# Kernel optimization log

Hardware: AMD Instinct MI355X
Metric: run time of the kernel (lower is better)

The kernel has to match this reference:

```python
import jax, jax.numpy as jnp
import numpy as np

BN_EPS = 1e-5
K = 16


def pairwise_sqdist(a, b):
    # a: (B,N,C), b: (B,M,C) -> (B,N,M)
    aa = jnp.sum(a * a, axis=-1)[:, :, None]
    bb = jnp.sum(b * b, axis=-1)[:, None, :]
    return aa + bb - 2.0 * jnp.einsum('bnc,bmc->bnm', a, b)


def knn_idx(pts, k):
    # pts: (B,N,C) -> (B,N,k) indices of k nearest points (incl. self)
    d = pairwise_sqdist(pts, pts)
    _, idx = jax.lax.top_k(-d, k)
    return idx


def gather_points(pts, idx):
    # pts: (B,N,C), idx: (B,N,k) -> (B,N,k,C)
    return jax.vmap(lambda p, i: p[i])(pts, idx)


def conv_bn(x, W, b, gm, bt, relu=True):
    # 1x1 Conv1d + BatchNorm1d (training-mode batch stats) [+ ReLU]
    # x: (B,Cin,N), W: (Cout,Cin)
    y = jnp.einsum('oc,bcn->bon', W, x) + b[None, :, None]
    mu = jnp.mean(y, axis=(0, 2), keepdims=True)
    var = jnp.var(y, axis=(0, 2), keepdims=True)
    y = (y - mu) / jnp.sqrt(var + BN_EPS) * gm[None, :, None] + bt[None, :, None]
    return jax.nn.relu(y) if relu else y


def graph_layer(x, W, b, gm, bt):
    # x: (B,C,N)
    ft = jnp.swapaxes(x, 1, 2)                # (B,N,C)
    idx = knn_idx(ft, K)                      # (B,N,k)
    knn_x = gather_points(ft, idx)            # (B,N,k,C)
    m = jnp.max(knn_x, axis=2)                # (B,N,C)
    return conv_bn(jnp.swapaxes(m, 1, 2), W, b, gm, bt, relu=True)


def setup_inputs() -> dict:
    key = jax.random.key(0)
    ks = jax.random.split(key, 8)
    B, N = 8, 2048
    d = {'x': jax.random.normal(ks[0], (B, N, 3), dtype=jnp.float32)}

    def conv_params(k, cout, cin):
        W = jax.random.normal(k, (cout, cin), dtype=jnp.float32) * 0.02
        return W, jnp.zeros((cout,), jnp.float32), jnp.ones((cout,), jnp.float32), jnp.zeros((cout,), jnp.float32)

    for name, k, co, ci in [('1', ks[1], 64, 12), ('2', ks[2], 64, 64), ('3', ks[3], 64, 64),
                            ('g1', ks[4], 128, 64), ('g2', ks[5], 1024, 128), ('4', ks[6], 512, 1024)]:
        W, b, gm, bt = conv_params(k, co, ci)
        d['W' + name] = W; d['b' + name] = b; d['gm' + name] = gm; d['bt' + name] = bt
    return d


def reference(x, W1, b1, gm1, bt1, W2, b2, gm2, bt2, W3, b3, gm3, bt3,
              Wg1, bg1, gmg1, btg1, Wg2, bg2, gmg2, btg2, W4, b4, gm4, bt4):
    # x: (B,N,3)
    idx = knn_idx(x, K)                       # (B,N,k)
    knn_x = gather_points(x, idx)             # (B,N,k,3)
    knn_x = knn_x - jnp.mean(knn_x, axis=2, keepdims=True)
    cov = jnp.einsum('bnkc,bnkd->bncd', knn_x, knn_x)      # (B,N,3,3)
    B, N = x.shape[0], x.shape[1]
    cov = cov.reshape(B, N, 9).transpose(0, 2, 1)          # (B,9,N)
    h = jnp.concatenate([jnp.swapaxes(x, 1, 2), cov], axis=1)  # (B,12,N)
    h = conv_bn(h, W1, b1, gm1, bt1)
    h = conv_bn(h, W2, b2, gm2, bt2)
    h = conv_bn(h, W3, b3, gm3, bt3)
    h = graph_layer(h, Wg1, bg1, gmg1, btg1)               # (B,128,N)
    h = graph_layer(h, Wg2, bg2, gmg2, btg2)               # (B,1024,N)
    h = conv_bn(h, W4, b4, gm4, bt4, relu=False)           # (B,512,N)
    return jnp.max(h, axis=-1)                             # (B,512)
```

## Files before the change

kernel.cpp:

```cpp
#include <hip/hip_runtime.h>
#include <math.h>

#define B_ 8
#define N_ 2048
#define KNN 16

typedef __attribute__((ext_vector_type(4))) float f32x4;
typedef __attribute__((ext_vector_type(8))) short bf16x8;
typedef __attribute__((ext_vector_type(8))) _Float16 f16x8;
typedef __attribute__((address_space(3))) unsigned int lds_u32_t;
typedef __attribute__((address_space(1))) const unsigned int glb_u32_t;

__device__ inline unsigned short f2bf(float f) {
    unsigned int x = __float_as_uint(f);
    unsigned int r = (x + 0x7fffu + ((x >> 16) & 1u)) >> 16;
    return (unsigned short)r;
}

__device__ inline unsigned int fflip(float f) {
    unsigned int u = __float_as_uint(f);
    return u ^ (0x80000000u | (unsigned int)((int)u >> 31));
}

__device__ inline unsigned long long shflx64(unsigned long long v, int m) {
    int lo = __shfl_xor((int)(unsigned int)(v & 0xffffffffull), m, 64);
    int hi = __shfl_xor((int)(unsigned int)(v >> 32), m, 64);
    return ((unsigned long long)(unsigned int)hi << 32) | (unsigned int)lo;
}

__device__ inline void ce(unsigned long long& a, unsigned long long& b) {
    bool c = a < b;
    unsigned long long lo = c ? a : b;
    unsigned long long hi = c ? b : a;
    a = lo;
    b = hi;
}

#define SORT16(q)                                                         \
    _Pragma("unroll") for (int kk_ = 2; kk_ <= 16; kk_ <<= 1)             \
    _Pragma("unroll") for (int jj_ = kk_ >> 1; jj_ > 0; jj_ >>= 1)        \
    _Pragma("unroll") for (int ii_ = 0; ii_ < 16; ii_++) {                \
        int ll_ = ii_ ^ jj_;                                              \
        if (ll_ > ii_) {                                                  \
            if ((ii_ & kk_) == 0) ce(q[ii_], q[ll_]);                     \
            else ce(q[ll_], q[ii_]);                                      \
        }                                                                 \
    }

#define MERGE16(q)                                                        \
    _Pragma("unroll") for (int jj_ = 8; jj_ > 0; jj_ >>= 1)               \
    _Pragma("unroll") for (int ii_ = 0; ii_ < 16; ii_++) {                \
        int ll_ = ii_ ^ jj_;                                              \
        if (ll_ > ii_) ce(q[ii_], q[ll_]);                                \
    }

#define TOP16OF32(kA, kB, q)                                              \
    SORT16(kA);                                                           \
    SORT16(kB);                                                           \
    _Pragma("unroll") for (int ii_ = 0; ii_ < 16; ii_++) {                \
        unsigned long long b_ = kB[15 - ii_];                             \
        q[ii_] = kA[ii_] < b_ ? kA[ii_] : b_;                             \
    }                                                                     \
    MERGE16(q);

#define EXTRACT16(q, op)                                                  \
    for (int r_ = 0; r_ < KNN; r_++) {                                    \
        unsigned long long mk_ = q[0];                                    \
        _Pragma("unroll") for (int s_ = 32; s_ > 0; s_ >>= 1) {           \
            unsigned long long ok_ = shflx64(mk_, s_);                    \
            if (ok_ < mk_) mk_ = ok_;                                     \
        }                                                                 \
        if (lane == 0) (op)[r_] = (int)(mk_ & 2047u);                     \
        bool pop_ = (q[0] == mk_);                                        \
        _Pragma("unroll") for (int t_ = 0; t_ < 15; t_++)                 \
            q[t_] = pop_ ? q[t_ + 1] : q[t_];                             \
        q[15] = pop_ ? ~0ull : q[15];                                     \
    }

__global__ __launch_bounds__(256, 4) void knn3_kernel(const float* __restrict__ x,
                                                      int* __restrict__ idx,
                                                      float* __restrict__ h0) {
    __shared__ float px[N_], py[N_], pz[N_];
    int b = blockIdx.y;
    const float* xb = x + (size_t)b * N_ * 3;
    for (int e = threadIdx.x; e < N_; e += 256) {
        px[e] = xb[e * 3 + 0];
        py[e] = xb[e * 3 + 1];
        pz[e] = xb[e * 3 + 2];
    }
    __syncthreads();

    int wave = threadIdx.x >> 6, lane = threadIdx.x & 63;
    int i = blockIdx.x * 4 + wave;
    float qx = px[i], qy = py[i], qz = pz[i];

    unsigned long long kA[16], kB[16];
#pragma unroll
    for (int t = 0; t < 16; t++) {
        int j = lane + t * 64;
        float dx = px[j] - qx, dy = py[j] - qy, dz = pz[j] - qz;
        float d = dx * dx + dy * dy + dz * dz;
        kA[t] = ((unsigned long long)fflip(d) << 11) | (unsigned int)j;
    }
#pragma unroll
    for (int t = 0; t < 16; t++) {
        int j = lane + (t + 16) * 64;
        float dx = px[j] - qx, dy = py[j] - qy, dz = pz[j] - qz;
        float d = dx * dx + dy * dy + dz * dz;
        kB[t] = ((unsigned long long)fflip(d) << 11) | (unsigned int)j;
    }

    unsigned long long q[16];
    TOP16OF32(kA, kB, q);

    int* op = idx + ((size_t)b * N_ + i) * KNN;
    unsigned int jr[16];
#pragma unroll
    for (int r_ = 0; r_ < KNN; r_++) {
        unsigned long long mk_ = q[0];
#pragma unroll
        for (int s_ = 32; s_ > 0; s_ >>= 1) {
            unsigned long long ok_ = shflx64(mk_, s_);
            if (ok_ < mk_) mk_ = ok_;
        }
        jr[r_] = (unsigned int)(mk_ & 2047u);
        if (lane == 0) op[r_] = (int)jr[r_];
        bool pop_ = (q[0] == mk_);
#pragma unroll
        for (int t_ = 0; t_ < 15; t_++) q[t_] = pop_ ? q[t_ + 1] : q[t_];
        q[15] = pop_ ? ~0ull : q[15];
    }

    float nx[16], ny[16], nz[16];
    float mx = 0.f, my = 0.f, mz = 0.f;
#pragma unroll
    for (int r_ = 0; r_ < 16; r_++) {
        int j = (int)jr[r_];
        nx[r_] = px[j]; ny[r_] = py[j]; nz[r_] = pz[j];
        mx += nx[r_]; my += ny[r_]; mz += nz[r_];
    }
    mx *= (1.f / KNN); my *= (1.f / KNN); mz *= (1.f / KNN);
    float c00 = 0, c01 = 0, c02 = 0, c11 = 0, c12 = 0, c22 = 0;
#pragma unroll
    for (int r_ = 0; r_ < 16; r_++) {
        float dx = nx[r_] - mx, dy = ny[r_] - my, dz = nz[r_] - mz;
        c00 += dx * dx; c01 += dx * dy; c02 += dx * dz;
        c11 += dy * dy; c12 += dy * dz; c22 += dz * dz;
    }
    if (lane == 0) {
        float* hb = h0 + (size_t)b * 12 * N_;
        hb[0 * N_ + i] = qx;
        hb[1 * N_ + i] = qy;
        hb[2 * N_ + i] = qz;
        hb[3 * N_ + i] = c00; hb[4 * N_ + i] = c01; hb[5 * N_ + i] = c02;
        hb[6 * N_ + i] = c01; hb[7 * N_ + i] = c11; hb[8 * N_ + i] = c12;
        hb[9 * N_ + i] = c02; hb[10 * N_ + i] = c12; hb[11 * N_ + i] = c22;
    }
}

__global__ __launch_bounds__(256) void gemm_kernel(const float* __restrict__ A,
                                                   const float* __restrict__ X,
                                                   const float* __restrict__ bias,
                                                   float* __restrict__ Y,
                                                   int O, int C) {
    __shared__ float Wt[16][132];
    __shared__ float Xt[16][132];
    const int N = N_;
    int b = blockIdx.z;
    int oB = blockIdx.y * 128, nB = blockIdx.x * 128;
    const float* Xb = X + (size_t)b * C * N;
    int tid = threadIdx.x;
    int tn = tid & 15, to = tid >> 4;

    float acc[8][8];
#pragma unroll
    for (int i = 0; i < 8; i++)
#pragma unroll
        for (int j = 0; j < 8; j++) acc[i][j] = 0.f;

    for (int c0 = 0; c0 < C; c0 += 16) {
#pragma unroll
        for (int r = 0; r < 8; r++) {
            int e = tid + r * 256;
            int k = e & 15, o = e >> 4;
            float v = 0.f;
            if (c0 + k < C && oB + o < O) v = A[(size_t)(oB + o) * C + c0 + k];
            Wt[k][o] = v;
        }
#pragma unroll
        for (int r = 0; r < 8; r++) {
            int e = tid + r * 256;
            int n = e & 127, k = e >> 7;
            float v = 0.f;
            if (c0 + k < C) v = Xb[(size_t)(c0 + k) * N + nB + n];
            Xt[k][n] = v;
        }
        __syncthreads();
#pragma unroll
        for (int k = 0; k < 16; k++) {
            float a[8], xv[8];
#pragma unroll
            for (int i = 0; i < 8; i++) a[i] = Wt[k][to * 8 + i];
#pragma unroll
            for (int m = 0; m < 4; m++) {
                xv[2 * m] = Xt[k][tn * 2 + 32 * m];
                xv[2 * m + 1] = Xt[k][tn * 2 + 32 * m + 1];
            }
#pragma unroll
            for (int i = 0; i < 8; i++)
#pragma unroll
                for (int j = 0; j < 8; j++) acc[i][j] = fmaf(a[i], xv[j], acc[i][j]);
        }
        __syncthreads();
    }

#pragma unroll
    for (int i = 0; i < 8; i++) {
        int o = oB + to * 8 + i;
        if (o >= O) continue;
        float bv = bias[o];
#pragma unroll
        for (int m = 0; m < 4; m++) {
            int n0 = nB + tn * 2 + 32 * m;
            float2 st = make_float2(acc[i][2 * m] + bv, acc[i][2 * m + 1] + bv);
            *reinterpret_cast<float2*>(&Y[((size_t)b * O + o) * N + n0]) = st;
        }
    }
}

__global__ __launch_bounds__(256) void splitbn_kernel(const float* __restrict__ y,
                                                      const float* __restrict__ scale,
                                                      const float* __restrict__ shift,
                                                      _Float16* __restrict__ fh,
                                                      _Float16* __restrict__ fl, int O) {
    __shared__ float tile[64][65];
    int b = blockIdx.z;
    int n0 = blockIdx.x * 64, o0 = blockIdx.y * 64;
    int t = threadIdx.x;
#pragma unroll
    for (int rr = 0; rr < 16; rr++) {
        int ol = rr * 4 + (t >> 6), nl = t & 63;
        float v = y[((size_t)b * O + o0 + ol) * N_ + n0 + nl];
        v = fmaf(v, scale[o0 + ol], shift[o0 + ol]);
        tile[ol][nl] = fmaxf(v, 0.f);
    }
    __syncthreads();
#pragma unroll
    for (int rr = 0; rr < 2; rr++) {
        int e = t + rr * 256;
        int n = e >> 3, og = (e & 7) * 8;
        f16x8 hv, lv;
#pragma unroll
        for (int j = 0; j < 8; j++) {
            float v = tile[og + j][n];
            _Float16 h = (_Float16)v;
            hv[j] = h;
            lv[j] = (_Float16)(v - (float)h);
        }
        size_t off = ((size_t)b * N_ + n0 + n) * O + o0 + og;
        *reinterpret_cast<uint4*>(&fh[off]) = *reinterpret_cast<uint4*>(&hv);
        *reinterpret_cast<uint4*>(&fl[off]) = *reinterpret_cast<uint4*>(&lv);
    }
}

__global__ __launch_bounds__(256) void normsh_kernel(const _Float16* __restrict__ fh,
                                                     const _Float16* __restrict__ fl,
                                                     float* __restrict__ nrm, int C) {
    int b = blockIdx.y;
    int i = blockIdx.x * 256 + threadIdx.x;
    const _Float16* ph = fh + ((size_t)(b << 11) + i) * C;
    const _Float16* pl = fl + ((size_t)(b << 11) + i) * C;
    float s = 0.f;
    for (int c = 0; c < C; c += 8) {
        f16x8 h = *reinterpret_cast<const f16x8*>(&ph[c]);
        f16x8 l = *reinterpret_cast<const f16x8*>(&pl[c]);
#pragma unroll
        for (int q = 0; q < 8; q++) {
            float v = (float)h[q] + (float)l[q];
            s = fmaf(v, v, s);
        }
    }
    nrm[(b << 11) + i] = s;
}

__global__ __launch_bounds__(256) void dmfma_kernel(const _Float16* __restrict__ Fh,
                                                    const _Float16* __restrict__ Fl,
                                                    const float* __restrict__ nrm,
                                                    float* __restrict__ D, int C) {
    __shared__ __align__(16) char smem[65536];
    _Float16* Ah = (_Float16*)(smem);
    _Float16* Al = (_Float16*)(smem + 16384);
    _Float16* Bh = (_Float16*)(smem + 32768);
    _Float16* Bl = (_Float16*)(smem + 49152);
    float(*Tt)[132] = (float(*)[132])smem;

    int bz = blockIdx.z;
    int t = blockIdx.x;
    int bx = (int)((sqrtf(8.f * (float)t + 1.f) - 1.f) * 0.5f);
    while ((bx + 1) * (bx + 2) / 2 <= t) bx++;
    while (bx * (bx + 1) / 2 > t) bx--;
    int by = t - bx * (bx + 1) / 2;
    int oB = by * 128, nB = bx * 128;
    const _Float16* Fhb = Fh + (size_t)bz * N_ * C;
    const _Float16* Flb = Fl + (size_t)bz * N_ * C;
    const float* nb = nrm + (size_t)bz * N_;
    float* Db = D + (size_t)bz * N_ * N_;

    int tid = threadIdx.x;
    int lane = tid & 63, w = tid >> 6;
    int wm = w & 1, wn = w >> 1;
    int lr = lane & 15, lg = lane >> 4;
    int lrow = lane >> 3;
    int lcol = ((lane & 7) ^ lrow) * 8;

    f32x4 acc[4][4];
#pragma unroll
    for (int m = 0; m < 4; m++)
#pragma unroll
        for (int n = 0; n < 4; n++) acc[m][n] = (f32x4){0.f, 0.f, 0.f, 0.f};

    for (int c0 = 0; c0 < C; c0 += 64) {
#pragma unroll
        for (int r = 0; r < 4; r++) {
            int seg = r * 4 + w;
            int row = seg * 8 + lrow;
            const _Float16* gah = &Fhb[(size_t)(oB + row) * C + c0 + lcol];
            const _Float16* gal = &Flb[(size_t)(oB + row) * C + c0 + lcol];
            const _Float16* gbh = &Fhb[(size_t)(nB + row) * C + c0 + lcol];
            const _Float16* gbl = &Flb[(size_t)(nB + row) * C + c0 + lcol];
            __builtin_amdgcn_global_load_lds((glb_u32_t*)gah, (lds_u32_t*)&Ah[seg * 512], 16, 0, 0);
            __builtin_amdgcn_global_load_lds((glb_u32_t*)gal, (lds_u32_t*)&Al[seg * 512], 16, 0, 0);
            __builtin_amdgcn_global_load_lds((glb_u32_t*)gbh, (lds_u32_t*)&Bh[seg * 512], 16, 0, 0);
            __builtin_amdgcn_global_load_lds((glb_u32_t*)gbl, (lds_u32_t*)&Bl[seg * 512], 16, 0, 0);
        }
        __syncthreads();
#pragma unroll
        for (int kk = 0; kk < 2; kk++) {
            f16x8 ah[4], al[4], bh[4], bl[4];
#pragma unroll
            for (int m = 0; m < 4; m++) {
                int row = wm * 64 + m * 16 + lr;
                int slot = (kk * 4 + lg) ^ (lr & 7);
                ah[m] = *reinterpret_cast<const f16x8*>(&Ah[row * 64 + slot * 8]);
                al[m] = *reinterpret_cast<const f16x8*>(&Al[row * 64 + slot * 8]);
            }
#pragma unroll
            for (int n = 0; n < 4; n++) {
                int row = wn * 64 + n * 16 + lr;
                int slot = (kk * 4 + lg) ^ (lr & 7);
                bh[n] = *reinterpret_cast<const f16x8*>(&Bh[row * 64 + slot * 8]);
                bl[n] = *reinterpret_cast<const f16x8*>(&Bl[row * 64 + slot * 8]);
            }
#pragma unroll
            for (int m = 0; m < 4; m++)
#pragma unroll
                for (int n = 0; n < 4; n++) {
                    acc[m][n] = __builtin_amdgcn_mfma_f32_16x16x32_f16(al[m], bh[n], acc[m][n], 0, 0, 0);
                    acc[m][n] = __builtin_amdgcn_mfma_f32_16x16x32_f16(ah[m], bl[n], acc[m][n], 0, 0, 0);
                    acc[m][n] = __builtin_amdgcn_mfma_f32_16x16x32_f16(ah[m], bh[n], acc[m][n], 0, 0, 0);
                }
        }
        __syncthreads();
    }

#pragma unroll
    for (int m = 0; m < 4; m++) {
#pragma unroll
        for (int r = 0; r < 4; r++) {
            int o = oB + wm * 64 + m * 16 + lg * 4 + r;
            float nr_ = nb[o];
#pragma unroll
            for (int n = 0; n < 4; n++) {
                int nv = nB + wn * 64 + n * 16 + lr;
                float val = nr_ + nb[nv] - 2.f * acc[m][n][r];
                unsigned int fk = fflip(val);
                Db[(size_t)o * N_ + nv] = __uint_as_float(fk);
                acc[m][n][r] = __uint_as_float(fk);
            }
        }
    }

    if (bx != by) {
        for (int p = 0; p < 4; p++) {
            __syncthreads();
            if (wm == (p >> 1)) {
#pragma unroll
                for (int mh = 0; mh < 2; mh++) {
                    int m = (p & 1) * 2 + mh;
                    int ib = m * 16 + lg * 4 - (p & 1) * 32;
#pragma unroll
                    for (int n = 0; n < 4; n++) {
                        int j = wn * 64 + n * 16 + lr;
#pragma unroll
                        for (int r = 0; r < 4; r++) Tt[ib + r][j] = acc[m][n][r];
                    }
                }
            }
            __syncthreads();
#pragma unroll
            for (int r = 0; r < 4; r++) {
                int e = tid + r * 256;
                int j = e >> 3, i4 = e & 7;
                float4 v;
                v.x = Tt[i4 * 4 + 0][j];
                v.y = Tt[i4 * 4 + 1][j];
                v.z = Tt[i4 * 4 + 2][j];
                v.w = Tt[i4 * 4 + 3][j];
                *reinterpret_cast<float4*>(&Db[(size_t)(nB + j) * N_ + oB + p * 32 + i4 * 4]) = v;
            }
        }
    }
}

template <int XLAYOUT, int FUSE, int DUALT>
__global__ __launch_bounds__(256, 4) void cgemm_kernel(const float* __restrict__ A,
                                                       const float* __restrict__ X,
                                                       const float* __restrict__ bias,
                                                       float* __restrict__ Y,
                                                       int O, int C,
                                                       const float* __restrict__ xs,
                                                       const float* __restrict__ xh,
                                                       float* __restrict__ Yt) {
    __shared__ float Wt[32][68];
    __shared__ float Xt[32][68];
    int b = blockIdx.z;
    int oB = blockIdx.y * 64, nB = blockIdx.x * 64;
    const float* Xb = X + (XLAYOUT == 0 ? (size_t)b * C * N_ : (size_t)b * N_ * C);
    int tid = threadIdx.x;
    int tn = tid & 15, to = tid >> 4;

    float acc[4][4];
#pragma unroll
    for (int i = 0; i < 4; i++)
#pragma unroll
        for (int j = 0; j < 4; j++) acc[i][j] = 0.f;

    for (int c0 = 0; c0 < C; c0 += 32) {
#pragma unroll
        for (int r = 0; r < 2; r++) {
            int e = tid + r * 256;
            int row = e >> 3, c4 = e & 7;
            float4 v = *reinterpret_cast<const float4*>(&A[(size_t)(oB + row) * C + c0 + c4 * 4]);
            Wt[c4 * 4 + 0][row] = v.x;
            Wt[c4 * 4 + 1][row] = v.y;
            Wt[c4 * 4 + 2][row] = v.z;
            Wt[c4 * 4 + 3][row] = v.w;
        }
        if (XLAYOUT == 0) {
#pragma unroll
            for (int r = 0; r < 2; r++) {
                int e = tid + r * 256;
                int k = e >> 4, n4 = e & 15;
                float4 v = *reinterpret_cast<const float4*>(&Xb[(size_t)(c0 + k) * N_ + nB + n4 * 4]);
                if (FUSE) {
                    float sc = xs[c0 + k], sh = xh[c0 + k];
                    v.x = fmaxf(fmaf(v.x, sc, sh), 0.f);
                    v.y = fmaxf(fmaf(v.y, sc, sh), 0.f);
                    v.z = fmaxf(fmaf(v.z, sc, sh), 0.f);
                    v.w = fmaxf(fmaf(v.w, sc, sh), 0.f);
                }
                *reinterpret_cast<float4*>(&Xt[k][n4 * 4]) = v;
            }
        } else {
#pragma unroll
            for (int r = 0; r < 2; r++) {
                int e = tid + r * 256;
                int n = e >> 3, c4 = e & 7;
                float4 v = *reinterpret_cast<const float4*>(&Xb[(size_t)(nB + n) * C + c0 + c4 * 4]);
                Xt[c4 * 4 + 0][n] = v.x;
                Xt[c4 * 4 + 1][n] = v.y;
                Xt[c4 * 4 + 2][n] = v.z;
                Xt[c4 * 4 + 3][n] = v.w;
            }
        }
        __syncthreads();
#pragma unroll
        for (int k = 0; k < 32; k++) {
            float a[4], xv[4];
            *reinterpret_cast<float4*>(&a[0]) = *reinterpret_cast<const float4*>(&Wt[k][to * 4]);
            *reinterpret_cast<float4*>(&xv[0]) = *reinterpret_cast<const float4*>(&Xt[k][tn * 4]);
#pragma unroll
            for (int i = 0; i < 4; i++)
#pragma unroll
                for (int j = 0; j < 4; j++) acc[i][j] = fmaf(a[i], xv[j], acc[i][j]);
        }
        __syncthreads();
    }

    float fin[4][4];
#pragma unroll
    for (int i = 0; i < 4; i++) {
        float bv = bias[oB + to * 4 + i];
#pragma unroll
        for (int j = 0; j < 4; j++) fin[i][j] = acc[i][j] + bv;
    }
#pragma unroll
    for (int i = 0; i < 4; i++) {
        int o = oB + to * 4 + i;
        int n0 = nB + tn * 4;
        float4 st;
        st.x = fin[i][0]; st.y = fin[i][1]; st.z = fin[i][2]; st.w = fin[i][3];
        *reinterpret_cast<float4*>(&Y[((size_t)b * O + o) * N_ + n0]) = st;
    }
    if (DUALT) {
#pragma unroll
        for (int j = 0; j < 4; j++) {
            int n = nB + tn * 4 + j;
            float4 st;
            st.x = fin[0][j]; st.y = fin[1][j]; st.z = fin[2][j]; st.w = fin[3][j];
            *reinterpret_cast<float4*>(&Yt[((size_t)b * N_ + n) * (size_t)O + oB + to * 4]) = st;
        }
    }
}

template <int EPI>
__global__ __launch_bounds__(256) void mgemm_kernel(const unsigned short* __restrict__ A,
                                                    const unsigned short* __restrict__ X,
                                                    const float* __restrict__ bias,
                                                    float* __restrict__ Y,
                                                    int O, int C,
                                                    float* __restrict__ part) {
    __shared__ unsigned short At[128 * 64];
    __shared__ unsigned short Bt[128 * 64];
    __shared__ float sred[2][2][64][4];
    int b = blockIdx.z;
    int oB = blockIdx.y * 128, nB = blockIdx.x * 128;
    const unsigned short* Xb = X + (size_t)b * N_ * C;
    int tid = threadIdx.x;
    int lane = tid & 63, w = tid >> 6;
    int wm = w & 1, wn = w >> 1;
    int lr = lane & 15, lg = lane >> 4;
    int lrow = lane >> 3;
    int lcol = ((lane & 7) ^ lrow) * 8;

    f32x4 acc[4][4];
#pragma unroll
    for (int m = 0; m < 4; m++)
#pragma unroll
        for (int n = 0; n < 4; n++) acc[m][n] = (f32x4){0.f, 0.f, 0.f, 0.f};

    for (int c0 = 0; c0 < C; c0 += 64) {
#pragma unroll
        for (int r = 0; r < 4; r++) {
            int seg = r * 4 + w;
            int row = seg * 8 + lrow;
            const unsigned short* ga = &A[(size_t)(oB + row) * C + c0 + lcol];
            const unsigned short* gb = &Xb[(size_t)(nB + row) * C + c0 + lcol];
            __builtin_amdgcn_global_load_lds((glb_u32_t*)ga, (lds_u32_t*)&At[seg * 512], 16, 0, 0);
            __builtin_amdgcn_global_load_lds((glb_u32_t*)gb, (lds_u32_t*)&Bt[seg * 512], 16, 0, 0);
        }
        __syncthreads();
#pragma unroll
        for (int kk = 0; kk < 2; kk++) {
            bf16x8 af[4], bfv[4];
#pragma unroll
            for (int m = 0; m < 4; m++) {
                int row = wm * 64 + m * 16 + lr;
                int slot = (kk * 4 + lg) ^ (lr & 7);
                af[m] = *reinterpret_cast<const bf16x8*>(&At[row * 64 + slot * 8]);
            }
#pragma unroll
            for (int n = 0; n < 4; n++) {
                int row = wn * 64 + n * 16 + lr;
                int slot = (kk * 4 + lg) ^ (lr & 7);
                bfv[n] = *reinterpret_cast<const bf16x8*>(&Bt[row * 64 + slot * 8]);
            }
#pragma unroll
            for (int m = 0; m < 4; m++)
#pragma unroll
                for (int n = 0; n < 4; n++)
                    acc[m][n] = __builtin_amdgcn_mfma_f32_16x16x32_bf16(af[m], bfv[n], acc[m][n], 0, 0, 0);
        }
        __syncthreads();
    }

    if (EPI == 1) {
#pragma unroll
        for (int m = 0; m < 4; m++) {
#pragma unroll
            for (int r = 0; r < 4; r++) {
                float v0 = acc[m][0][r], v1 = acc[m][1][r];
                float v2 = acc[m][2][r], v3 = acc[m][3][r];
                float mx = fmaxf(fmaxf(v0, v1), fmaxf(v2, v3));
                float mn = fminf(fminf(v0, v1), fminf(v2, v3));
                float s = (v0 + v1) + (v2 + v3);
                float s2 = fmaf(v0, v0, fmaf(v1, v1, fmaf(v2, v2, v3 * v3)));
#pragma unroll
                for (int msk = 1; msk <= 8; msk <<= 1) {
                    mx = fmaxf(mx, __shfl_xor(mx, msk, 64));
                    mn = fminf(mn, __shfl_xor(mn, msk, 64));
                    s += __shfl_xor(s, msk, 64);
                    s2 += __shfl_xor(s2, msk, 64);
                }
                if (lr == 0) {
                    int ol = m * 16 + lg * 4 + r;
                    sred[wm][wn][ol][0] = mx;
                    sred[wm][wn][ol][1] = mn;
                    sred[wm][wn][ol][2] = s;
                    sred[wm][wn][ol][3] = s2;
                }
            }
        }
        __syncthreads();
        if (tid < 128) {
            int wmv = tid >> 6, ol = tid & 63;
            float mx = fmaxf(sred[wmv][0][ol][0], sred[wmv][1][ol][0]);
            float mn = fminf(sred[wmv][0][ol][1], sred[wmv][1][ol][1]);
            float s = sred[wmv][0][ol][2] + sred[wmv][1][ol][2];
            float s2 = sred[wmv][0][ol][3] + sred[wmv][1][ol][3];
            int o = oB + wmv * 64 + ol;
            float* pp = &part[((size_t)(o * 8 + b) * 16 + blockIdx.x) * 4];
            pp[0] = mx; pp[1] = mn; pp[2] = s; pp[3] = s2;
        }
    } else {
#pragma unroll
        for (int m = 0; m < 4; m++) {
            int o0 = oB + wm * 64 + m * 16 + lg * 4;
            float4 bv = *reinterpret_cast<const float4*>(&bias[o0]);
            float s[4] = {0.f, 0.f, 0.f, 0.f};
            float s2[4] = {0.f, 0.f, 0.f, 0.f};
#pragma unroll
            for (int n = 0; n < 4; n++) {
                int nv = nB + wn * 64 + n * 16 + lr;
                float4 st;
                st.x = acc[m][n][0] + bv.x;
                st.y = acc[m][n][1] + bv.y;
                st.z = acc[m][n][2] + bv.z;
                st.w = acc[m][n][3] + bv.w;
                *reinterpret_cast<float4*>(&Y[((size_t)b * N_ + nv) * (size_t)O + o0]) = st;
                s[0] += st.x; s2[0] = fmaf(st.x, st.x, s2[0]);
                s[1] += st.y; s2[1] = fmaf(st.y, st.y, s2[1]);
                s[2] += st.z; s2[2] = fmaf(st.z, st.z, s2[2]);
                s[3] += st.w; s2[3] = fmaf(st.w, st.w, s2[3]);
            }
#pragma unroll
            for (int r = 0; r < 4; r++) {
#pragma unroll
                for (int msk = 1; msk <= 8; msk <<= 1) {
                    s[r] += __shfl_xor(s[r], msk, 64);
                    s2[r] += __shfl_xor(s2[r], msk, 64);
                }
                if (lr == 0) {
                    int ol = m * 16 + lg * 4 + r;
                    sred[wm][wn][ol][0] = s[r];
                    sred[wm][wn][ol][1] = s2[r];
                }
            }
        }
        __syncthreads();
        if (tid < 128) {
            int wmv = tid >> 6, ol = tid & 63;
            float s = sred[wmv][0][ol][0] + sred[wmv][1][ol][0];
            float s2 = sred[wmv][0][ol][1] + sred[wmv][1][ol][1];
            int o = oB + wmv * 64 + ol;
            float* pp = &part[((size_t)(o * 8 + b) * 16 + blockIdx.x) * 2];
            pp[0] = s; pp[1] = s2;
        }
    }
}

__global__ __launch_bounds__(128) void bnfin_kernel(const float* __restrict__ part,
                                                    const float* __restrict__ gm,
                                                    const float* __restrict__ bt,
                                                    float* __restrict__ scale,
                                                    float* __restrict__ shift) {
    int o = blockIdx.x;
    int t = threadIdx.x;
    const float* p = &part[((size_t)(o * 8 + (t >> 4)) * 16 + (t & 15)) * 2];
    float s = p[0], s2 = p[1];
#pragma unroll
    for (int msk = 1; msk <= 32; msk <<= 1) {
        s += __shfl_xor(s, msk, 64);
        s2 += __shfl_xor(s2, msk, 64);
    }
    __shared__ float red[4];
    int wv = t >> 6, lane = t & 63;
    if (lane == 0) { red[wv] = s; red[2 + wv] = s2; }
    __syncthreads();
    if (t == 0) {
        float S = red[0] + red[1], S2 = red[2] + red[3];
        float mu = S * (1.f / (B_ * N_));
        float var = S2 * (1.f / (B_ * N_)) - mu * mu;
        float inv = 1.f / sqrtf(var + 1e-5f);
        float sc = gm[o] * inv;
        scale[o] = sc;
        shift[o] = fmaf(-mu, sc, bt[o]);
    }
}

__global__ __launch_bounds__(256) void applycvt_kernel(const float* __restrict__ yt,
                                                       const float* __restrict__ scale,
                                                       const float* __restrict__ shift,
                                                       unsigned short* __restrict__ outh) {
    size_t i = ((size_t)blockIdx.x * 256 + threadIdx.x) * 8;
    int o = (int)(i & 1023u);
    float4 a = *reinterpret_cast<const float4*>(&yt[i]);
    float4 c = *reinterpret_cast<const float4*>(&yt[i + 4]);
    float4 s0 = *reinterpret_cast<const float4*>(&scale[o]);
    float4 s1 = *reinterpret_cast<const float4*>(&scale[o + 4]);
    float4 h0 = *reinterpret_cast<const float4*>(&shift[o]);
    float4 h1 = *reinterpret_cast<const float4*>(&shift[o + 4]);
    unsigned short u[8];
    u[0] = f2bf(fmaxf(fmaf(a.x, s0.x, h0.x), 0.f));
    u[1] = f2bf(fmaxf(fmaf(a.y, s0.y, h0.y), 0.f));
    u[2] = f2bf(fmaxf(fmaf(a.z, s0.z, h0.z), 0.f));
    u[3] = f2bf(fmaxf(fmaf(a.w, s0.w, h0.w), 0.f));
    u[4] = f2bf(fmaxf(fmaf(c.x, s1.x, h1.x), 0.f));
    u[5] = f2bf(fmaxf(fmaf(c.y, s1.y, h1.y), 0.f));
    u[6] = f2bf(fmaxf(fmaf(c.z, s1.z, h1.z), 0.f));
    u[7] = f2bf(fmaxf(fmaf(c.w, s1.w, h1.w), 0.f));
    uint4 pk;
    pk.x = (unsigned)u[0] | ((unsigned)u[1] << 16);
    pk.y = (unsigned)u[2] | ((unsigned)u[3] << 16);
    pk.z = (unsigned)u[4] | ((unsigned)u[5] << 16);
    pk.w = (unsigned)u[6] | ((unsigned)u[7] << 16);
    *reinterpret_cast<uint4*>(&outh[i]) = pk;
}

__global__ __launch_bounds__(128) void bnmax_kernel(const float* __restrict__ part,
                                                    const float* __restrict__ gm,
                                                    const float* __restrict__ bt,
                                                    float* __restrict__ out) {
    int o = blockIdx.x;
    int t = threadIdx.x;
    int b = t >> 4, nb = t & 15;
    const float* p = &part[((size_t)(o * 8 + b) * 16 + nb) * 4];
    float mx = p[0], mn = p[1], s = p[2], s2 = p[3];

    float ss = s, ss2 = s2;
#pragma unroll
    for (int msk = 1; msk <= 32; msk <<= 1) {
        ss += __shfl_xor(ss, msk, 64);
        ss2 += __shfl_xor(ss2, msk, 64);
    }
    __shared__ float red[4];
    int wv = t >> 6, lane = t & 63;
    if (lane == 0) { red[wv] = ss; red[2 + wv] = ss2; }
    __syncthreads();
    float S = red[0] + red[1], S2 = red[2] + red[3];
    float mu = S * (1.f / (B_ * N_));
    float var = S2 * (1.f / (B_ * N_)) - mu * mu;
    float inv = 1.f / sqrtf(var + 1e-5f);
    float sc = gm[o] * inv;
    float sh = fmaf(-mu, sc, bt[o]);

#pragma unroll
    for (int msk = 1; msk <= 8; msk <<= 1) {
        mx = fmaxf(mx, __shfl_xor(mx, msk, 64));
        mn = fminf(mn, __shfl_xor(mn, msk, 64));
    }
    if (nb == 0) out[b * 512 + o] = fmaf(sc, sc >= 0.f ? mx : mn, sh);
}

__global__ __launch_bounds__(256) void bnstats_kernel(const float* __restrict__ y,
                                                      const float* __restrict__ gm,
                                                      const float* __restrict__ bt,
                                                      float* __restrict__ scale,
                                                      float* __restrict__ shift, int O) {
    int o = blockIdx.x;
    float s = 0.f, s2 = 0.f;
    for (int e = threadIdx.x; e < B_ * N_; e += 256) {
        int b = e >> 11, n = e & (N_ - 1);
        float v = y[((size_t)b * O + o) * N_ + n];
        s += v;
        s2 = fmaf(v, v, s2);
    }
#pragma unroll
    for (int off = 32; off; off >>= 1) {
        s += __shfl_down(s, off, 64);
        s2 += __shfl_down(s2, off, 64);
    }
    __shared__ float red[8];
    int lane = threadIdx.x & 63, w = threadIdx.x >> 6;
    if (lane == 0) { red[w] = s; red[4 + w] = s2; }
    __syncthreads();
    if (threadIdx.x == 0) {
        s = red[0] + red[1] + red[2] + red[3];
        s2 = red[4] + red[5] + red[6] + red[7];
        float mu = s * (1.f / (B_ * N_));
        float var = s2 * (1.f / (B_ * N_)) - mu * mu;
        float inv = 1.f / sqrtf(var + 1e-5f);
        float sc = gm[o] * inv;
        scale[o] = sc;
        shift[o] = fmaf(-mu, sc, bt[o]);
    }
}

__global__ __launch_bounds__(256, 4) void topk_kernel(const float* __restrict__ D,
                                                      int* __restrict__ idx) {
    int wave = threadIdx.x >> 6, lane = threadIdx.x & 63;
    int i = blockIdx.x * 4 + wave;
    const unsigned int* dp = (const unsigned int*)(D + (size_t)i * N_);

    unsigned long long kA[16], kB[16];
#pragma unroll
    for (int t = 0; t < 4; t++) {
        uint4 v = *reinterpret_cast<const uint4*>(&dp[t * 256 + lane * 4]);
        int j0 = t * 256 + lane * 4;
        kA[t * 4 + 0] = ((unsigned long long)v.x << 11) | (unsigned int)(j0 + 0);
        kA[t * 4 + 1] = ((unsigned long long)v.y << 11) | (unsigned int)(j0 + 1);
        kA[t * 4 + 2] = ((unsigned long long)v.z << 11) | (unsigned int)(j0 + 2);
        kA[t * 4 + 3] = ((unsigned long long)v.w << 11) | (unsigned int)(j0 + 3);
    }
#pragma unroll
    for (int t = 4; t < 8; t++) {
        uint4 v = *reinterpret_cast<const uint4*>(&dp[t * 256 + lane * 4]);
        int j0 = t * 256 + lane * 4;
        kB[(t - 4) * 4 + 0] = ((unsigned long long)v.x << 11) | (unsigned int)(j0 + 0);
        kB[(t - 4) * 4 + 1] = ((unsigned long long)v.y << 11) | (unsigned int)(j0 + 1);
        kB[(t - 4) * 4 + 2] = ((unsigned long long)v.z << 11) | (unsigned int)(j0 + 2);
        kB[(t - 4) * 4 + 3] = ((unsigned long long)v.w << 11) | (unsigned int)(j0 + 3);
    }

    unsigned long long q[16];
    TOP16OF32(kA, kB, q);

    int* op = idx + (size_t)i * KNN;
    EXTRACT16(q, op);
}

__global__ __launch_bounds__(256) void gathermax_kernel(const float* __restrict__ ftraw,
                                                        const int* __restrict__ idx,
                                                        const float* __restrict__ scale,
                                                        const float* __restrict__ shift,
                                                        float* __restrict__ out, int cLog) {
    int C = 1 << cLog;
    int b = blockIdx.y;
    int nb = (blockIdx.x << (8 - cLog)) + (threadIdx.x >> cLog);
    int c = threadIdx.x & (C - 1);
    float sc = scale[c], sh = shift[c];
    const int* ip = idx + (((size_t)b << 11) + nb) * KNN;
    float m = -3.4e38f;
#pragma unroll
    for (int k = 0; k < KNN; k++) {
        int j = ip[k];
        float v = ftraw[(((size_t)b << 11) + j) * C + c];
        m = fmaxf(m, fmaxf(fmaf(v, sc, sh), 0.f));
    }
    out[(((size_t)b << 11) + nb) * C + c] = m;
}

__global__ __launch_bounds__(256) void gmaxh2_kernel(const float* __restrict__ ftraw,
                                                     const int* __restrict__ idx,
                                                     const float* __restrict__ scale,
                                                     const float* __restrict__ shift,
                                                     unsigned short* __restrict__ out) {
    const int C = 128;
    int b = blockIdx.y;
    int nb = blockIdx.x * 16 + (threadIdx.x >> 4);
    int cc = (threadIdx.x & 15) * 8;
    float4 s0 = *reinterpret_cast<const float4*>(&scale[cc]);
    float4 s1 = *reinterpret_cast<const float4*>(&scale[cc + 4]);
    float4 h0 = *reinterpret_cast<const float4*>(&shift[cc]);
    float4 h1 = *reinterpret_cast<const float4*>(&shift[cc + 4]);
    const int* ip = idx + (((size_t)b << 11) + nb) * KNN;
    float m[8];
#pragma unroll
    for (int q = 0; q < 8; q++) m[q] = -3.4e38f;
#pragma unroll
    for (int k = 0; k < KNN; k++) {
        int j = ip[k];
        const float* p = &ftraw[(((size_t)b << 11) + j) * C + cc];
        float4 a = *reinterpret_cast<const float4*>(p);
        float4 c2 = *reinterpret_cast<const float4*>(p + 4);
        m[0] = fmaxf(m[0], fmaxf(fmaf(a.x, s0.x, h0.x), 0.f));
        m[1] = fmaxf(m[1], fmaxf(fmaf(a.y, s0.y, h0.y), 0.f));
        m[2] = fmaxf(m[2], fmaxf(fmaf(a.z, s0.z, h0.z), 0.f));
        m[3] = fmaxf(m[3], fmaxf(fmaf(a.w, s0.w, h0.w), 0.f));
        m[4] = fmaxf(m[4], fmaxf(fmaf(c2.x, s1.x, h1.x), 0.f));
        m[5] = fmaxf(m[5], fmaxf(fmaf(c2.y, s1.y, h1.y), 0.f));
        m[6] = fmaxf(m[6], fmaxf(fmaf(c2.z, s1.z, h1.z), 0.f));
        m[7] = fmaxf(m[7], fmaxf(fmaf(c2.w, s1.w, h1.w), 0.f));
    }
    unsigned short u[8];
#pragma unroll
    for (int q = 0; q < 8; q++) u[q] = f2bf(m[q]);
    uint4 pk;
    pk.x = (unsigned)u[0] | ((unsigned)u[1] << 16);
    pk.y = (unsigned)u[2] | ((unsigned)u[3] << 16);
    pk.z = (unsigned)u[4] | ((unsigned)u[5] << 16);
    pk.w = (unsigned)u[6] | ((unsigned)u[7] << 16);
    *reinterpret_cast<uint4*>(&out[(((size_t)b << 11) + nb) * C + cc]) = pk;
}

__global__ __launch_bounds__(256) void wcvt2_kernel(const float* __restrict__ w1,
                                                    unsigned short* __restrict__ o1, int c1,
                                                    const float* __restrict__ w2,
                                                    unsigned short* __restrict__ o2, int c2) {
    int i = blockIdx.x * 256 + threadIdx.x;
    if (i < c1) o1[i] = f2bf(w1[i]);
    else if (i < c1 + c2) o2[i - c1] = f2bf(w2[i - c1]);
}

extern "C" void kernel_launch(void* const* d_in, const int* in_sizes, int n_in,
                              void* d_out, int out_size, void* d_ws, size_t ws_size,
                              hipStream_t stream) {
    const float* x = (const float*)d_in[0];
    const float* W1 = (const float*)d_in[1];
    const float* b1 = (const float*)d_in[2];
    const float* gm1 = (const float*)d_in[3];
    const float* bt1 = (const float*)d_in[4];
    const float* W2 = (const float*)d_in[5];
    const float* b2 = (const float*)d_in[6];
    const float* gm2 = (const float*)d_in[7];
    const float* bt2 = (const float*)d_in[8];
    const float* W3 = (const float*)d_in[9];
    const float* b3 = (const float*)d_in[10];
    const float* gm3 = (const float*)d_in[11];
    const float* bt3 = (const float*)d_in[12];
    const float* Wg1 = (const float*)d_in[13];
    const float* bg1 = (const float*)d_in[14];
    const float* gmg1 = (const float*)d_in[15];
    const float* btg1 = (const float*)d_in[16];
    const float* Wg2 = (const float*)d_in[17];
    const float* bg2 = (const float*)d_in[18];
    const float* gmg2 = (const float*)d_in[19];
    const float* btg2 = (const float*)d_in[20];
    const float* W4 = (const float*)d_in[21];
    const float* b4 = (const float*)d_in[22];
    const float* gm4 = (const float*)d_in[23];
    const float* bt4 = (const float*)d_in[24];
    float* out = (float*)d_out;
    (void)b4;

    if (ws_size < 154214400ull) return;
    char* base = (char*)d_ws;
    float* scale = (float*)(base + 0);
    float* shift = (float*)(base + 4096);
    float* nrm = (float*)(base + 8192);
    int* idx = (int*)(base + 73728);
    unsigned short* Wg2h = (unsigned short*)(base + 1122304);
    unsigned short* W4h = (unsigned short*)(base + 1384448);
    _Float16* Fh1 = (_Float16*)(base + 2433024);
    _Float16* Fl1 = (_Float16*)(base + 4530176);
    _Float16* Fh2 = (_Float16*)(base + 6627328);
    _Float16* Fl2 = (_Float16*)(base + 10821632);
    float* bufD4 = (float*)(base + 19210240);
    float* bufLt = (float*)(base + 19210240);
    unsigned short* bufLh = (unsigned short*)(base + 86319104);
    char* E = base + 119873536;
    float* h0 = (float*)(E + 0);
    float* bufA = (float*)(E + 786432);
    float* bufB = (float*)(E + 4980736);
    float* bufC = (float*)(E + 9175040);
    float* bufM1 = (float*)(E + 13369344);
    float* bufM2 = (float*)(E + 21757952);
    unsigned short* bufM3h = (unsigned short*)(E + 30146560);
    float* part = (float*)(E + 0);

    wcvt2_kernel<<<2560, 256, 0, stream>>>(Wg2, Wg2h, 1024 * 128, W4, W4h, 512 * 1024);

    knn3_kernel<<<dim3(512, 8), 256, 0, stream>>>(x, idx, h0);

    gemm_kernel<<<dim3(16, 1, 8), 256, 0, stream>>>(W1, h0, b1, bufA, 64, 12);
    bnstats_kernel<<<64, 256, 0, stream>>>(bufA, gm1, bt1, scale, shift, 64);

    cgemm_kernel<0, 1, 0><<<dim3(32, 1, 8), 256, 0, stream>>>(W2, bufA, b2, bufB, 64, 64, scale, shift, nullptr);
    bnstats_kernel<<<64, 256, 0, stream>>>(bufB, gm2, bt2, scale, shift, 64);

    cgemm_kernel<0, 1, 1><<<dim3(32, 1, 8), 256, 0, stream>>>(W3, bufB, b3, bufA, 64, 64, scale, shift, bufC);
    bnstats_kernel<<<64, 256, 0, stream>>>(bufA, gm3, bt3, scale, shift, 64);

    splitbn_kernel<<<dim3(32, 1, 8), 256, 0, stream>>>(bufA, scale, shift, Fh1, Fl1, 64);
    normsh_kernel<<<dim3(8, 8), 256, 0, stream>>>(Fh1, Fl1, nrm, 64);
    for (int c = 0; c < 2; c++) {
        dmfma_kernel<<<dim3(136, 1, 4), 256, 0, stream>>>(
            Fh1 + (size_t)c * 4 * N_ * 64, Fl1 + (size_t)c * 4 * N_ * 64,
            nrm + (size_t)c * 4 * N_, bufD4, 64);
        topk_kernel<<<2048, 256, 0, stream>>>(bufD4, idx + (size_t)c * 4 * N_ * KNN);
    }
    gathermax_kernel<<<dim3(512, 8), 256, 0, stream>>>(bufC, idx, scale, shift, bufB, 6);

    cgemm_kernel<1, 0, 1><<<dim3(32, 2, 8), 256, 0, stream>>>(Wg1, bufB, bg1, bufM1, 128, 64, nullptr, nullptr, bufM2);
    bnstats_kernel<<<128, 256, 0, stream>>>(bufM1, gmg1, btg1, scale, shift, 128);

    splitbn_kernel<<<dim3(32, 2, 8), 256, 0, stream>>>(bufM1, scale, shift, Fh2, Fl2, 128);
    normsh_kernel<<<dim3(8, 8), 256, 0, stream>>>(Fh2, Fl2, nrm, 128);
    for (int c = 0; c < 2; c++) {
        dmfma_kernel<<<dim3(136, 1, 4), 256, 0, stream>>>(
            Fh2 + (size_t)c * 4 * N_ * 128, Fl2 + (size_t)c * 4 * N_ * 128,
            nrm + (size_t)c * 4 * N_, bufD4, 128);
        topk_kernel<<<2048, 256, 0, stream>>>(bufD4, idx + (size_t)c * 4 * N_ * KNN);
    }
    gmaxh2_kernel<<<dim3(128, 8), 256, 0, stream>>>(bufM2, idx, scale, shift, bufM3h);

    mgemm_kernel<2><<<dim3(16, 8, 8), 256, 0, stream>>>(Wg2h, bufM3h, bg2, bufLt, 1024, 128, part);
    bnfin_kernel<<<1024, 128, 0, stream>>>(part, gmg2, btg2, scale, shift);
    applycvt_kernel<<<8192, 256, 0, stream>>>(bufLt, scale, shift, bufLh);

    mgemm_kernel<1><<<dim3(16, 4, 8), 256, 0, stream>>>(W4h, bufLh, nullptr, nullptr, 512, 1024, part);
    bnmax_kernel<<<512, 128, 0, stream>>>(part, gm4, bt4, out);
}
```

Baseline: 515.6 us.

## Fuse BN partial statistics into GEMM epilogues and batch first kNN distance pass

The GEMM and cgemm epilogues now emit per-block partial sums and sums of squares, and small finalize kernels (bnfin, new bnfin32) replace the bnstats kernels that reread the whole output. The first graph layer's distance GEMM and top-k now run once over all 8 batches instead of in two halves of 4, using a larger D buffer, and bufC moves to a new workspace region to make room. This removes full-tensor rereads for batch-norm statistics and two kernel launches, at the cost of more workspace and extra shuffles in the epilogues.

```diff
diff --git a/kernel.cpp b/kernel.cpp
--- a/kernel.cpp
+++ b/kernel.cpp
@@ -162,7 +162,8 @@
                                                    const float* __restrict__ X,
                                                    const float* __restrict__ bias,
                                                    float* __restrict__ Y,
-                                                   int O, int C) {
+                                                   int O, int C,
+                                                   float* __restrict__ part) {
     __shared__ float Wt[16][132];
     __shared__ float Xt[16][132];
     const int N = N_;
@@ -219,11 +220,23 @@
         int o = oB + to * 8 + i;
         if (o >= O) continue;
         float bv = bias[o];
+        float s = 0.f, s2 = 0.f;
 #pragma unroll
         for (int m = 0; m < 4; m++) {
             int n0 = nB + tn * 2 + 32 * m;
-            float2 st = make_float2(acc[i][2 * m] + bv, acc[i][2 * m + 1] + bv);
-            *reinterpret_cast<float2*>(&Y[((size_t)b * O + o) * N + n0]) = st;
+            float v0 = acc[i][2 * m] + bv, v1 = acc[i][2 * m + 1] + bv;
+            *reinterpret_cast<float2*>(&Y[((size_t)b * O + o) * N + n0]) = make_float2(v0, v1);
+            s += v0 + v1;
+            s2 = fmaf(v0, v0, fmaf(v1, v1, s2));
+        }
+#pragma unroll
+        for (int msk = 1; msk <= 8; msk <<= 1) {
+            s += __shfl_xor(s, msk, 64);
+            s2 += __shfl_xor(s2, msk, 64);
+        }
+        if (tn == 0) {
+            float* pp = &part[((size_t)(o * 8 + b) * 16 + blockIdx.x) * 2];
+            pp[0] = s; pp[1] = s2;
         }
     }
 }
@@ -420,7 +433,8 @@
                                                        int O, int C,
                                                        const float* __restrict__ xs,
                                                        const float* __restrict__ xh,
-                                                       float* __restrict__ Yt) {
+                                                       float* __restrict__ Yt,
+                                                       float* __restrict__ part) {
     __shared__ float Wt[32][68];
     __shared__ float Xt[32][68];
     int b = blockIdx.z;
@@ -509,6 +523,22 @@
             float4 st;
             st.x = fin[0][j]; st.y = fin[1][j]; st.z = fin[2][j]; st.w = fin[3][j];
             *reinterpret_cast<float4*>(&Yt[((size_t)b * N_ + n) * (size_t)O + oB + to * 4]) = st;
+        }
+    }
+#pragma unroll
+    for (int i = 0; i < 4; i++) {
+        float s = (fin[i][0] + fin[i][1]) + (fin[i][2] + fin[i][3]);
+        float s2 = fmaf(fin[i][0], fin[i][0], fmaf(fin[i][1], fin[i][1],
+                   fmaf(fin[i][2], fin[i][2], fin[i][3] * fin[i][3])));
+#pragma unroll
+        for (int msk = 1; msk <= 8; msk <<= 1) {
+            s += __shfl_xor(s, msk, 64);
+            s2 += __shfl_xor(s2, msk, 64);
+        }
+        if (tn == 0) {
+            int o = oB + to * 4 + i;
+            float* pp = &part[((size_t)(o * 8 + b) * 32 + blockIdx.x) * 2];
+            pp[0] = s; pp[1] = s2;
         }
     }
 }
@@ -679,6 +709,36 @@
     __syncthreads();
     if (t == 0) {
         float S = red[0] + red[1], S2 = red[2] + red[3];
+        float mu = S * (1.f / (B_ * N_));
+        float var = S2 * (1.f / (B_ * N_)) - mu * mu;
+        float inv = 1.f / sqrtf(var + 1e-5f);
+        float sc = gm[o] * inv;
+        scale[o] = sc;
+        shift[o] = fmaf(-mu, sc, bt[o]);
+    }
+}
+
+__global__ __launch_bounds__(256) void bnfin32_kernel(const float* __restrict__ part,
+                                                      const float* __restrict__ gm,
+                                                      const float* __restrict__ bt,
+                                                      float* __restrict__ scale,
+                                                      float* __restrict__ shift) {
+    int o = blockIdx.x;
+    int t = threadIdx.x;
+    const float* p = &part[((size_t)(o * 8 + (t >> 5)) * 32 + (t & 31)) * 2];
+    float s = p[0], s2 = p[1];
+#pragma unroll
+    for (int msk = 1; msk <= 32; msk <<= 1) {
+        s += __shfl_xor(s, msk, 64);
+        s2 += __shfl_xor(s2, msk, 64);
+    }
+    __shared__ float red[8];
+    int wv = t >> 6, lane = t & 63;
+    if (lane == 0) { red[wv] = s; red[4 + wv] = s2; }
+    __syncthreads();
+    if (t == 0) {
+        float S = (red[0] + red[1]) + (red[2] + red[3]);
+        float S2 = (red[4] + red[5]) + (red[6] + red[7]);
         float mu = S * (1.f / (B_ * N_));
         float var = S2 * (1.f / (B_ * N_)) - mu * mu;
         float inv = 1.f / sqrtf(var + 1e-5f);
@@ -750,40 +810,6 @@
         mn = fminf(mn, __shfl_xor(mn, msk, 64));
     }
     if (nb == 0) out[b * 512 + o] = fmaf(sc, sc >= 0.f ? mx : mn, sh);
-}
-
-__global__ __launch_bounds__(256) void bnstats_kernel(const float* __restrict__ y,
-                                                      const float* __restrict__ gm,
-                                                      const float* __restrict__ bt,
-                                                      float* __restrict__ scale,
-                                                      float* __restrict__ shift, int O) {
-    int o = blockIdx.x;
-    float s = 0.f, s2 = 0.f;
-    for (int e = threadIdx.x; e < B_ * N_; e += 256) {
-        int b = e >> 11, n = e & (N_ - 1);
-        float v = y[((size_t)b * O + o) * N_ + n];
-        s += v;
-        s2 = fmaf(v, v, s2);
-    }
-#pragma unroll
-    for (int off = 32; off; off >>= 1) {
-        s += __shfl_down(s, off, 64);
-        s2 += __shfl_down(s2, off, 64);
-    }
-    __shared__ float red[8];
-    int lane = threadIdx.x & 63, w = threadIdx.x >> 6;
-    if (lane == 0) { red[w] = s; red[4 + w] = s2; }
-    __syncthreads();
-    if (threadIdx.x == 0) {
-        s = red[0] + red[1] + red[2] + red[3];
-        s2 = red[4] + red[5] + red[6] + red[7];
-        float mu = s * (1.f / (B_ * N_));
-        float var = s2 * (1.f / (B_ * N_)) - mu * mu;
-        float inv = 1.f / sqrtf(var + 1e-5f);
-        float sc = gm[o] * inv;
-        scale[o] = sc;
-        shift[o] = fmaf(-mu, sc, bt[o]);
-    }
 }
 
 __global__ __launch_bounds__(256, 4) void topk_kernel(const float* __restrict__ D,
@@ -928,6 +954,7 @@
     float* scale = (float*)(base + 0);
     float* shift = (float*)(base + 4096);
     float* nrm = (float*)(base + 8192);
+    float* partC1 = (float*)(base + 8192);
     int* idx = (int*)(base + 73728);
     unsigned short* Wg2h = (unsigned short*)(base + 1122304);
     unsigned short* W4h = (unsigned short*)(base + 1384448);
@@ -935,14 +962,16 @@
     _Float16* Fl1 = (_Float16*)(base + 4530176);
     _Float16* Fh2 = (_Float16*)(base + 6627328);
     _Float16* Fl2 = (_Float16*)(base + 10821632);
+    float* bufC = (float*)(base + 15015936);
+    float* bufD8 = (float*)(base + 19210240);
     float* bufD4 = (float*)(base + 19210240);
     float* bufLt = (float*)(base + 19210240);
     unsigned short* bufLh = (unsigned short*)(base + 86319104);
     char* E = base + 119873536;
+    float* partC = (float*)(E + 0);
     float* h0 = (float*)(E + 0);
     float* bufA = (float*)(E + 786432);
     float* bufB = (float*)(E + 4980736);
-    float* bufC = (float*)(E + 9175040);
     float* bufM1 = (float*)(E + 13369344);
     float* bufM2 = (float*)(E + 21757952);
     unsigned short* bufM3h = (unsigned short*)(E + 30146560);
@@ -952,27 +981,23 @@
 
     knn3_kernel<<<dim3(512, 8), 256, 0, stream>>>(x, idx, h0);
 
-    gemm_kernel<<<dim3(16, 1, 8), 256, 0, stream>>>(W1, h0, b1, bufA, 64, 12);
-    bnstats_kernel<<<64, 256, 0, stream>>>(bufA, gm1, bt1, scale, shift, 64);
-
-    cgemm_kernel<0, 1, 0><<<dim3(32, 1, 8), 256, 0, stream>>>(W2, bufA, b2, bufB, 64, 64, scale, shift, nullptr);
-    bnstats_kernel<<<64, 256, 0, stream>>>(bufB, gm2, bt2, scale, shift, 64);
-
-    cgemm_kernel<0, 1, 1><<<dim3(32, 1, 8), 256, 0, stream>>>(W3, bufB, b3, bufA, 64, 64, scale, shift, bufC);
-    bnstats_kernel<<<64, 256, 0, stream>>>(bufA, gm3, bt3, scale, shift, 64);
+    gemm_kernel<<<dim3(16, 1, 8), 256, 0, stream>>>(W1, h0, b1, bufA, 64, 12, partC1);
+    bnfin_kernel<<<64, 128, 0, stream>>>(partC1, gm1, bt1, scale, shift);
+
+    cgemm_kernel<0, 1, 0><<<dim3(32, 1, 8), 256, 0, stream>>>(W2, bufA, b2, bufB, 64, 64, scale, shift, nullptr, partC);
+    bnfin32_kernel<<<64, 256, 0, stream>>>(partC, gm2, bt2, scale, shift);
+
+    cgemm_kernel<0, 1, 1><<<dim3(32, 1, 8), 256, 0, stream>>>(W3, bufB, b3, bufA, 64, 64, scale, shift, bufC, partC);
+    bnfin32_kernel<<<64, 256, 0, stream>>>(partC, gm3, bt3, scale, shift);
 
     splitbn_kernel<<<dim3(32, 1, 8), 256, 0, stream>>>(bufA, scale, shift, Fh1, Fl1, 64);
     normsh_kernel<<<dim3(8, 8), 256, 0, stream>>>(Fh1, Fl1, nrm, 64);
-    for (int c = 0; c < 2; c++) {
-        dmfma_kernel<<<dim3(136, 1, 4), 256, 0, stream>>>(
-            Fh1 + (size_t)c * 4 * N_ * 64, Fl1 + (size_t)c * 4 * N_ * 64,
-            nrm + (size_t)c * 4 * N_, bufD4, 64);
-        topk_kernel<<<2048, 256, 0, stream>>>(bufD4, idx + (size_t)c * 4 * N_ * KNN);
-    }
+    dmfma_kernel<<<dim3(136, 1, 8), 256, 0, stream>>>(Fh1, Fl1, nrm, bufD8, 64);
+    topk_kernel<<<4096, 256, 0, stream>>>(bufD8, idx);
     gathermax_kernel<<<dim3(512, 8), 256, 0, stream>>>(bufC, idx, scale, shift, bufB, 6);
 
-    cgemm_kernel<1, 0, 1><<<dim3(32, 2, 8), 256, 0, stream>>>(Wg1, bufB, bg1, bufM1, 128, 64, nullptr, nullptr, bufM2);
-    bnstats_kernel<<<128, 256, 0, stream>>>(bufM1, gmg1, btg1, scale, shift, 128);
+    cgemm_kernel<1, 0, 1><<<dim3(32, 2, 8), 256, 0, stream>>>(Wg1, bufB, bg1, bufM1, 128, 64, nullptr, nullptr, bufM2, partC);
+    bnfin32_kernel<<<128, 256, 0, stream>>>(partC, gmg1, btg1, scale, shift);
 
     splitbn_kernel<<<dim3(32, 2, 8), 256, 0, stream>>>(bufM1, scale, shift, Fh2, Fl2, 128);
     normsh_kernel<<<dim3(8, 8), 256, 0, stream>>>(Fh2, Fl2, nrm, 128);
```

Result: faster. 438.7 us (-14.9%).
